# Kernel tuning notes

Hardware: AMD Instinct MI355X
Metric: run time of the kernel (lower is better)

The kernel has to match this reference:

```python
import jax, jax.numpy as jnp
import numpy as np

N = 50000      # nodes
E = 800000     # edges (avg degree 16)
D = 128        # node_dim
H = 128        # hidden_dim
ED = 16        # edge_dim (unused by GCNConv, kept for signature fidelity)
G = 64         # graphs in batch
EPS = 1e-5     # BatchNorm eps


def setup_inputs() -> dict:
    key = jax.random.key(0)
    ks = jax.random.split(key, 16)
    s = 0.05
    inp = {
        "x": jax.random.normal(ks[0], (N, D), jnp.float32),
        "edge_index": jax.random.randint(ks[1], (2, E), 0, N, dtype=jnp.int64),
        "edge_attr": jax.random.normal(ks[2], (E, ED), jnp.float32),
        "batch": jnp.sort(jax.random.randint(ks[3], (N,), 0, G, dtype=jnp.int64)),
        # GCNConv weights/biases
        "W1": jax.random.normal(ks[4], (D, H), jnp.float32) * s,
        "b1": jnp.zeros((H,), jnp.float32),
        "W2": jax.random.normal(ks[5], (H, H), jnp.float32) * s,
        "b2": jnp.zeros((H,), jnp.float32),
        "W3": jax.random.normal(ks[6], (H, H), jnp.float32) * s,
        "b3": jnp.zeros((H,), jnp.float32),
        # BatchNorm affine params (training-mode batch stats)
        "g1": jnp.ones((H,), jnp.float32), "be1": jnp.zeros((H,), jnp.float32),
        "g2": jnp.ones((H,), jnp.float32), "be2": jnp.zeros((H,), jnp.float32),
        "g3": jnp.ones((H,), jnp.float32), "be3": jnp.zeros((H,), jnp.float32),
    }
    return inp


def reference(x, edge_index, edge_attr, batch,
              W1, b1, W2, b2, W3, b3,
              g1, be1, g2, be2, g3, be3):
    n = x.shape[0]
    src, dst = edge_index[0], edge_index[1]

    # GCN symmetric normalization with added self-loops:
    # deg[i] = 1 + in_degree(i); norm(e) = deg[src]^-1/2 * deg[dst]^-1/2
    deg = jax.ops.segment_sum(jnp.ones((src.shape[0],), x.dtype), dst,
                              num_segments=n) + 1.0
    dinv = jax.lax.rsqrt(deg)
    edge_norm = (dinv[src] * dinv[dst])[:, None]   # [E,1]
    self_norm = (dinv * dinv)[:, None]             # [N,1] self-loop weight

    def gcn(h, W, b):
        h = h @ W                                  # [N,H]
        agg = jax.ops.segment_sum(h[src] * edge_norm, dst, num_segments=n)
        return agg + h * self_norm + b

    def bn_sigmoid(h, g, b):
        m = h.mean(0)
        v = jnp.mean(jnp.square(h - m), 0)         # biased variance (torch BN)
        return jax.nn.sigmoid((h - m) * jax.lax.rsqrt(v + EPS) * g + b)

    h = bn_sigmoid(gcn(x, W1, b1), g1, be1)
    h = bn_sigmoid(gcn(h, W2, b2), g2, be2)
    h = bn_sigmoid(gcn(h, W3, b3), g3, be3)

    # global_mean_pool over graph ids
    cnt = jax.ops.segment_sum(jnp.ones((n,), h.dtype), batch, num_segments=G)
    pooled = jax.ops.segment_sum(h, batch, num_segments=G)
    return pooled / jnp.maximum(cnt, 1.0)[:, None]
```

## Files before the change

### kernel.cpp

```cpp
#include <hip/hip_runtime.h>
#include <math.h>

#define NDIM 128

typedef __attribute__((ext_vector_type(8))) short short8;
typedef __attribute__((ext_vector_type(4))) float f32x4;

__device__ __forceinline__ float sigmoidf_(float x){ return 1.0f/(1.0f + __expf(-x)); }

__device__ __forceinline__ unsigned short f2bf(float f){
  unsigned u = __float_as_uint(f);
  unsigned r = (u + 0x7fffu + ((u >> 16) & 1u)) >> 16;
  return (unsigned short)r;
}

__global__ void deg_count_k(const int* __restrict__ dst, int* __restrict__ counts, int E){
  int e = blockIdx.x*blockDim.x + threadIdx.x;
  if(e < E) atomicAdd(&counts[dst[e]], 1);
}

__global__ void scan1_k(const int* __restrict__ counts, int* __restrict__ scanned,
                        int* __restrict__ chunksums, int N){
  __shared__ int lds[256];
  int t = threadIdx.x; int idx = blockIdx.x*256 + t;
  int x = (idx < N) ? counts[idx] : 0;
  lds[t] = x; __syncthreads();
  for(int o=1;o<256;o<<=1){
    int v = (t>=o) ? lds[t-o] : 0;
    __syncthreads();
    lds[t] += v;
    __syncthreads();
  }
  if(idx < N) scanned[idx] = lds[t];
  if(t == 255) chunksums[blockIdx.x] = lds[255];
}

__global__ void scan2_k(int* __restrict__ chunksums, int nchunks){
  __shared__ int lds[256];
  int t = threadIdx.x;
  int x = (t < nchunks) ? chunksums[t] : 0;
  lds[t] = x; __syncthreads();
  for(int o=1;o<256;o<<=1){
    int v = (t>=o) ? lds[t-o] : 0;
    __syncthreads();
    lds[t] += v;
    __syncthreads();
  }
  if(t < nchunks) chunksums[t] = lds[t] - x;
}

__global__ void scan3_k(const int* __restrict__ scanned, const int* __restrict__ counts,
                        const int* __restrict__ chunksums, int* __restrict__ row_start,
                        float* __restrict__ dinv, int N){
  int i = blockIdx.x*blockDim.x + threadIdx.x;
  if(i < N){
    row_start[i] = scanned[i] - counts[i] + chunksums[i>>8];
    dinv[i] = rsqrtf(1.0f + (float)counts[i]);
  }
}

__global__ void fill_k(const int* __restrict__ src, const int* __restrict__ dst,
                       const int* __restrict__ row_start,
                       int* __restrict__ cursor, unsigned short* __restrict__ csr, int E){
  int e = blockIdx.x*blockDim.x + threadIdx.x;
  if(e >= E) return;
  int d = dst[e];
  int pos = row_start[d] + atomicAdd(&cursor[d], 1);
  csr[pos] = (unsigned short)src[e];
}

__global__ void wprep_k(const float* __restrict__ W0, const float* __restrict__ W1,
                        const float* __restrict__ W2, unsigned short* __restrict__ Wsw,
                        const int* __restrict__ batch, int* __restrict__ bound,
                        int N, int G){
  int t = blockIdx.x*256 + threadIdx.x;
  if(t < 3*16384){
    int l = t >> 14; int i = t & 16383;
    const float* W = (l==0) ? W0 : ((l==1) ? W1 : W2);
    int k = i >> 7, n = i & 127;
    Wsw[l*16384 + (((k>>3)*128 + n)<<3) + (k&7)] = f2bf(W[k*128+n]);
  } else {
    int g = t - 3*16384;
    if(g <= G){
      int lo = 0, hi = N;
      while(lo < hi){ int mid = (lo+hi)>>1; if(batch[mid] < g) lo = mid+1; else hi = mid; }
      bound[g] = lo;
    }
  }
}

__global__ __launch_bounds__(256) void gemm_mfma_k(const float* __restrict__ A,
                                                   const unsigned short* __restrict__ Wsw,
                                                   unsigned short* __restrict__ Bh,
                                                   const float* __restrict__ dinv,
                                                   const float* __restrict__ sums,
                                                   const float* __restrict__ sumsq,
                                                   const float* __restrict__ gam,
                                                   const float* __restrict__ bet,
                                                   int N){
  __shared__ unsigned short Al[16384];
  __shared__ unsigned short Wl[16384];
  __shared__ float scl[NDIM], shl[NDIM], dvl[NDIM];
  int t = threadIdx.x;
  int row0 = blockIdx.x * 128;
  bool bn = (sums != nullptr);

  if(bn && t < NDIM){
    float invN = 1.0f/(float)N;
    float m = sums[t]*invN;
    float var = fmaxf(sumsq[t]*invN - m*m, 0.f);
    float s = gam[t]*rsqrtf(var + 1e-5f);
    scl[t] = s; shl[t] = bet[t] - m*s;
  }
  __syncthreads();

  if(t < NDIM){
    int r = row0 + t;
    dvl[t] = (r < N) ? dinv[r] : 0.f;
  }
  #pragma unroll
  for(int i=0;i<8;i++){
    int u = t + i*256;
    *(uint4*)&Wl[u<<3] = *(const uint4*)&Wsw[u<<3];
  }
  int o = t & 15, rbase = t >> 4;
  #pragma unroll
  for(int it=0; it<8; it++){
    int r = rbase + it*16;
    int grow = row0 + r;
    float4 v0 = make_float4(0.f,0.f,0.f,0.f), v1 = v0;
    if(grow < N){
      v0 = *(const float4*)&A[grow*NDIM + o*8];
      v1 = *(const float4*)&A[grow*NDIM + o*8 + 4];
      if(bn){
        float4 sc0 = *(const float4*)&scl[o*8],   sh0 = *(const float4*)&shl[o*8];
        float4 sc1 = *(const float4*)&scl[o*8+4], sh1 = *(const float4*)&shl[o*8+4];
        v0.x = sigmoidf_(v0.x*sc0.x + sh0.x); v0.y = sigmoidf_(v0.y*sc0.y + sh0.y);
        v0.z = sigmoidf_(v0.z*sc0.z + sh0.z); v0.w = sigmoidf_(v0.w*sc0.w + sh0.w);
        v1.x = sigmoidf_(v1.x*sc1.x + sh1.x); v1.y = sigmoidf_(v1.y*sc1.y + sh1.y);
        v1.z = sigmoidf_(v1.z*sc1.z + sh1.z); v1.w = sigmoidf_(v1.w*sc1.w + sh1.w);
      }
    }
    uint4 pk;
    pk.x = (unsigned)f2bf(v0.x) | ((unsigned)f2bf(v0.y)<<16);
    pk.y = (unsigned)f2bf(v0.z) | ((unsigned)f2bf(v0.w)<<16);
    pk.z = (unsigned)f2bf(v1.x) | ((unsigned)f2bf(v1.y)<<16);
    pk.w = (unsigned)f2bf(v1.z) | ((unsigned)f2bf(v1.w)<<16);
    *(uint4*)&Al[(o*128 + r)<<3] = pk;
  }
  __syncthreads();

  int wv = t >> 6, lane = t & 63, quad = lane >> 4, l16 = lane & 15;
  int rw = (wv & 1) * 64, cw = (wv >> 1) * 64;
  f32x4 acc[4][4];
  #pragma unroll
  for(int rt=0;rt<4;rt++)
    #pragma unroll
    for(int ct=0;ct<4;ct++) acc[rt][ct] = (f32x4){0.f,0.f,0.f,0.f};

  #pragma unroll
  for(int ks=0; ks<4; ks++){
    short8 a[4], b[4];
    #pragma unroll
    for(int rt=0;rt<4;rt++)
      a[rt] = *(short8*)&Al[(((ks*4+quad)*128) + rw + rt*16 + l16) << 3];
    #pragma unroll
    for(int ct=0;ct<4;ct++)
      b[ct] = *(short8*)&Wl[(((ks*4+quad)*128) + cw + ct*16 + l16) << 3];
    #pragma unroll
    for(int rt=0;rt<4;rt++)
      #pragma unroll
      for(int ct=0;ct<4;ct++)
        acc[rt][ct] = __builtin_amdgcn_mfma_f32_16x16x32_bf16(a[rt], b[ct], acc[rt][ct], 0, 0, 0);
  }

  #pragma unroll
  for(int rt=0;rt<4;rt++){
    int lr = rw + rt*16 + quad*4;
    int gr = row0 + lr;
    #pragma unroll
    for(int reg=0;reg<4;reg++){
      float dv = dvl[lr + reg];
      if(gr + reg < N){
        #pragma unroll
        for(int ct=0;ct<4;ct++){
          int col = cw + ct*16 + l16;
          Bh[(gr+reg)*NDIM + col] = f2bf(acc[rt][ct][reg]*dv);
        }
      }
    }
  }
}

__global__ void agg_k(const unsigned int* __restrict__ hb,
                      const float* __restrict__ dinv,
                      const int* __restrict__ row_start, const int* __restrict__ counts,
                      const unsigned short* __restrict__ csr,
                      const float* __restrict__ bias, float* __restrict__ hC, int N){
  int i = blockIdx.x;
  if(i >= N) return;
  int lane = threadIdx.x;
  int rs = row_start[i], re = rs + counts[i];
  float ax = 0.f, ay = 0.f;
  int j = rs;
  for(; j+7 < re; j += 8){
    int s0=csr[j],   s1=csr[j+1], s2=csr[j+2], s3=csr[j+3];
    int s4=csr[j+4], s5=csr[j+5], s6=csr[j+6], s7=csr[j+7];
    unsigned u0 = hb[(size_t)s0*64 + lane];
    unsigned u1 = hb[(size_t)s1*64 + lane];
    unsigned u2 = hb[(size_t)s2*64 + lane];
    unsigned u3 = hb[(size_t)s3*64 + lane];
    unsigned u4 = hb[(size_t)s4*64 + lane];
    unsigned u5 = hb[(size_t)s5*64 + lane];
    unsigned u6 = hb[(size_t)s6*64 + lane];
    unsigned u7 = hb[(size_t)s7*64 + lane];
    ax += __uint_as_float(u0<<16) + __uint_as_float(u1<<16)
        + __uint_as_float(u2<<16) + __uint_as_float(u3<<16)
        + __uint_as_float(u4<<16) + __uint_as_float(u5<<16)
        + __uint_as_float(u6<<16) + __uint_as_float(u7<<16);
    ay += __uint_as_float(u0 & 0xffff0000u) + __uint_as_float(u1 & 0xffff0000u)
        + __uint_as_float(u2 & 0xffff0000u) + __uint_as_float(u3 & 0xffff0000u)
        + __uint_as_float(u4 & 0xffff0000u) + __uint_as_float(u5 & 0xffff0000u)
        + __uint_as_float(u6 & 0xffff0000u) + __uint_as_float(u7 & 0xffff0000u);
  }
  for(; j < re; j++){
    int s0 = csr[j];
    unsigned u0 = hb[(size_t)s0*64 + lane];
    ax += __uint_as_float(u0<<16);
    ay += __uint_as_float(u0 & 0xffff0000u);
  }
  float di = dinv[i];
  unsigned su = hb[(size_t)i*64 + lane];
  float2 bv = *(const float2*)&bias[lane*2];
  float2 o;
  o.x = di*(ax + __uint_as_float(su<<16))           + bv.x;
  o.y = di*(ay + __uint_as_float(su & 0xffff0000u)) + bv.y;
  *(float2*)&hC[(size_t)i*NDIM + lane*2] = o;
}

__global__ void stats_k(const float* __restrict__ h, float* __restrict__ sums,
                        float* __restrict__ sumsq, int N){
  __shared__ float ls[256], lq[256];
  int t = threadIdx.x;
  int f = t & 127, half = t >> 7;
  int rowsPerBlock = (N + gridDim.x - 1)/gridDim.x;
  int r0 = blockIdx.x * rowsPerBlock;
  int r1 = min(N, r0 + rowsPerBlock);
  float s=0.f, q=0.f;
  for(int r=r0+half; r<r1; r+=2){
    float v = h[r*NDIM + f];
    s += v; q += v*v;
  }
  ls[t]=s; lq[t]=q; __syncthreads();
  if(t < 128){
    s = ls[t] + ls[t+128];
    q = lq[t] + lq[t+128];
    atomicAdd(&sums[f], s);
    atomicAdd(&sumsq[f], q);
  }
}

#define PCH 128
__global__ __launch_bounds__(256) void pool_k(const float* __restrict__ hC,
                                              const int* __restrict__ batch,
                                              const float* __restrict__ sums,
                                              const float* __restrict__ sumsq,
                                              const float* __restrict__ gam,
                                              const float* __restrict__ bet,
                                              float* __restrict__ out, int N){
  __shared__ float scl[NDIM], shl[NDIM];
  int t = threadIdx.x;
  if(t < NDIM){
    float invN = 1.0f/(float)N;
    float m = sums[t]*invN;
    float var = fmaxf(sumsq[t]*invN - m*m, 0.f);
    float s = gam[t]*rsqrtf(var + 1e-5f);
    scl[t] = s; shl[t] = bet[t] - m*s;
  }
  __syncthreads();
  int f = t & 127, half = t >> 7;
  int r0 = blockIdx.x*PCH + half;
  int r1 = min(N, blockIdx.x*PCH + PCH);
  float sc = scl[f], sh = shl[f];
  float acc = 0.f; int cur = -1;
  for(int r = r0; r < r1; r += 2){
    int g = batch[r];
    if(g != cur){
      if(cur >= 0) atomicAdd(&out[cur*NDIM + f], acc);
      acc = 0.f; cur = g;
    }
    acc += sigmoidf_(hC[r*NDIM + f]*sc + sh);
  }
  if(cur >= 0) atomicAdd(&out[cur*NDIM + f], acc);
}

__global__ void div_k(float* __restrict__ out, const int* __restrict__ bound){
  int g = blockIdx.x, f = threadIdx.x;
  float cnt = (float)(bound[g+1] - bound[g]);
  out[g*NDIM + f] /= fmaxf(cnt, 1.0f);
}

extern "C" void kernel_launch(void* const* d_in, const int* in_sizes, int n_in,
                              void* d_out, int out_size, void* d_ws, size_t ws_size,
                              hipStream_t stream){
  const float* x     = (const float*)d_in[0];
  const int*   ei    = (const int*)d_in[1];
  const int*   batch = (const int*)d_in[3];
  const float* W [3] = {(const float*)d_in[4], (const float*)d_in[6], (const float*)d_in[8]};
  const float* bi[3] = {(const float*)d_in[5], (const float*)d_in[7], (const float*)d_in[9]};
  const float* gg[3] = {(const float*)d_in[10], (const float*)d_in[12], (const float*)d_in[14]};
  const float* bb[3] = {(const float*)d_in[11], (const float*)d_in[13], (const float*)d_in[15]};

  int N = in_sizes[0] / NDIM;
  int E = in_sizes[1] / 2;
  int G = out_size / NDIM;
  const int* src = ei;
  const int* dst = ei + E;

  char* p = (char*)d_ws;
  auto alloc = [&](size_t bytes)->void*{
    void* r = (void*)p; p += (bytes + 255) & ~(size_t)255; return r;
  };
  unsigned short* hB  = (unsigned short*)alloc((size_t)N*NDIM*2);
  unsigned short* Wsw = (unsigned short*)alloc(3*16384*2);
  float* hC        = (float*)alloc((size_t)N*NDIM*4);
  int*   counts    = (int*)  alloc((size_t)2*N*4);
  int*   cursor    = counts + N;
  int*   scanned   = (int*)  alloc((size_t)N*4);
  int*   chunksums = (int*)  alloc(256*4);
  int*   row_start = (int*)  alloc((size_t)N*4);
  float* dinv      = (float*)alloc((size_t)N*4);
  unsigned short* csr = (unsigned short*)alloc((size_t)E*2);
  float* sums      = (float*)alloc(2*3*128*4);
  float* sumsq     = sums + 3*128;
  int*   bound     = (int*)  alloc(256*4);

  hipMemsetAsync(counts, 0, (size_t)2*N*4, stream);
  hipMemsetAsync(sums,  0, 2*3*128*4, stream);
  hipMemsetAsync(d_out, 0, (size_t)out_size*4, stream);

  deg_count_k<<<(E+255)/256, 256, 0, stream>>>(dst, counts, E);

  int nchunks = (N+255)/256;
  scan1_k<<<nchunks, 256, 0, stream>>>(counts, scanned, chunksums, N);
  scan2_k<<<1, 256, 0, stream>>>(chunksums, nchunks);
  scan3_k<<<(N+255)/256, 256, 0, stream>>>(scanned, counts, chunksums, row_start, dinv, N);
  fill_k<<<(E+255)/256, 256, 0, stream>>>(src, dst, row_start, cursor, csr, E);
  wprep_k<<<(3*16384+256+255)/256, 256, 0, stream>>>(W[0], W[1], W[2], Wsw, batch, bound, N, G);

  const float* hin = x;
  for(int l=0; l<3; l++){
    const float* sm = (l == 0) ? nullptr : (sums  + (l-1)*128);
    const float* sq = (l == 0) ? nullptr : (sumsq + (l-1)*128);
    const float* gm = (l == 0) ? nullptr : gg[l-1];
    const float* be = (l == 0) ? nullptr : bb[l-1];
    gemm_mfma_k<<<(N+127)/128, 256, 0, stream>>>(hin, Wsw + l*16384, hB, dinv,
                                                 sm, sq, gm, be, N);
    agg_k<<<N, 64, 0, stream>>>((const unsigned int*)hB, dinv, row_start, counts,
                                csr, bi[l], hC, N);
    stats_k<<<400, 256, 0, stream>>>(hC, sums + l*128, sumsq + l*128, N);
    hin = hC;
  }

  pool_k<<<(N+PCH-1)/PCH, 256, 0, stream>>>(hC, batch, sums + 2*128, sumsq + 2*128,
                                            gg[2], bb[2], (float*)d_out, N);
  div_k<<<G, 128, 0, stream>>>((float*)d_out, bound);
}
```

Before: 475.7 us.

## Store aggregated activations as bf16 and build CSR with precomputed edge ranks

The aggregation output hC changes from fp32 to packed bf16, which halves the bytes written by agg_k and read by stats_k, gemm (layers 2-3) and pool_k. CSR construction now records each edge's atomic rank during degree counting, so the fill pass writes directly without a second atomic on a cursor array. This costs an extra E-sized rank buffer, and the pre-BatchNorm values lose precision, which affects the batch statistics and the downstream results.

```diff
diff --git a/kernel.cpp b/kernel.cpp
--- a/kernel.cpp
+++ b/kernel.cpp
@@ -13,10 +13,13 @@
   unsigned r = (u + 0x7fffu + ((u >> 16) & 1u)) >> 16;
   return (unsigned short)r;
 }
-
-__global__ void deg_count_k(const int* __restrict__ dst, int* __restrict__ counts, int E){
+__device__ __forceinline__ float bflo(unsigned u){ return __uint_as_float(u<<16); }
+__device__ __forceinline__ float bfhi(unsigned u){ return __uint_as_float(u & 0xffff0000u); }
+
+__global__ void pass1_k(const int* __restrict__ dst, int* __restrict__ counts,
+                        int* __restrict__ rank, int E){
   int e = blockIdx.x*blockDim.x + threadIdx.x;
-  if(e < E) atomicAdd(&counts[dst[e]], 1);
+  if(e < E) rank[e] = atomicAdd(&counts[dst[e]], 1);
 }
 
 __global__ void scan1_k(const int* __restrict__ counts, int* __restrict__ scanned,
@@ -59,14 +62,12 @@
   }
 }
 
-__global__ void fill_k(const int* __restrict__ src, const int* __restrict__ dst,
-                       const int* __restrict__ row_start,
-                       int* __restrict__ cursor, unsigned short* __restrict__ csr, int E){
+__global__ void pass2_k(const int* __restrict__ src, const int* __restrict__ dst,
+                        const int* __restrict__ rank, const int* __restrict__ row_start,
+                        unsigned short* __restrict__ csr, int E){
   int e = blockIdx.x*blockDim.x + threadIdx.x;
   if(e >= E) return;
-  int d = dst[e];
-  int pos = row_start[d] + atomicAdd(&cursor[d], 1);
-  csr[pos] = (unsigned short)src[e];
+  csr[row_start[dst[e]] + rank[e]] = (unsigned short)src[e];
 }
 
 __global__ void wprep_k(const float* __restrict__ W0, const float* __restrict__ W1,
@@ -89,7 +90,7 @@
   }
 }
 
-__global__ __launch_bounds__(256) void gemm_mfma_k(const float* __restrict__ A,
+__global__ __launch_bounds__(256) void gemm_mfma_k(const void* __restrict__ Avoid,
                                                    const unsigned short* __restrict__ Wsw,
                                                    unsigned short* __restrict__ Bh,
                                                    const float* __restrict__ dinv,
@@ -112,8 +113,6 @@
     float s = gam[t]*rsqrtf(var + 1e-5f);
     scl[t] = s; shl[t] = bet[t] - m*s;
   }
-  __syncthreads();
-
   if(t < NDIM){
     int r = row0 + t;
     dvl[t] = (r < N) ? dinv[r] : 0.f;
@@ -123,30 +122,53 @@
     int u = t + i*256;
     *(uint4*)&Wl[u<<3] = *(const uint4*)&Wsw[u<<3];
   }
+  __syncthreads();
+
   int o = t & 15, rbase = t >> 4;
-  #pragma unroll
-  for(int it=0; it<8; it++){
-    int r = rbase + it*16;
-    int grow = row0 + r;
-    float4 v0 = make_float4(0.f,0.f,0.f,0.f), v1 = v0;
-    if(grow < N){
-      v0 = *(const float4*)&A[grow*NDIM + o*8];
-      v1 = *(const float4*)&A[grow*NDIM + o*8 + 4];
-      if(bn){
-        float4 sc0 = *(const float4*)&scl[o*8],   sh0 = *(const float4*)&shl[o*8];
-        float4 sc1 = *(const float4*)&scl[o*8+4], sh1 = *(const float4*)&shl[o*8+4];
-        v0.x = sigmoidf_(v0.x*sc0.x + sh0.x); v0.y = sigmoidf_(v0.y*sc0.y + sh0.y);
-        v0.z = sigmoidf_(v0.z*sc0.z + sh0.z); v0.w = sigmoidf_(v0.w*sc0.w + sh0.w);
-        v1.x = sigmoidf_(v1.x*sc1.x + sh1.x); v1.y = sigmoidf_(v1.y*sc1.y + sh1.y);
-        v1.z = sigmoidf_(v1.z*sc1.z + sh1.z); v1.w = sigmoidf_(v1.w*sc1.w + sh1.w);
+  if(bn){
+    const unsigned* Ab = (const unsigned*)Avoid;
+    #pragma unroll
+    for(int it=0; it<8; it++){
+      int r = rbase + it*16;
+      int grow = row0 + r;
+      uint4 pk = {0,0,0,0};
+      if(grow < N){
+        uint4 pb = *(const uint4*)&Ab[(size_t)grow*64 + o*4];
+        float a0=bflo(pb.x), a1=bfhi(pb.x), a2=bflo(pb.y), a3=bfhi(pb.y);
+        float a4=bflo(pb.z), a5=bfhi(pb.z), a6=bflo(pb.w), a7=bfhi(pb.w);
+        int f = o*8;
+        a0 = sigmoidf_(a0*scl[f+0] + shl[f+0]);
+        a1 = sigmoidf_(a1*scl[f+1] + shl[f+1]);
+        a2 = sigmoidf_(a2*scl[f+2] + shl[f+2]);
+        a3 = sigmoidf_(a3*scl[f+3] + shl[f+3]);
+        a4 = sigmoidf_(a4*scl[f+4] + shl[f+4]);
+        a5 = sigmoidf_(a5*scl[f+5] + shl[f+5]);
+        a6 = sigmoidf_(a6*scl[f+6] + shl[f+6]);
+        a7 = sigmoidf_(a7*scl[f+7] + shl[f+7]);
+        pk.x = (unsigned)f2bf(a0) | ((unsigned)f2bf(a1)<<16);
+        pk.y = (unsigned)f2bf(a2) | ((unsigned)f2bf(a3)<<16);
+        pk.z = (unsigned)f2bf(a4) | ((unsigned)f2bf(a5)<<16);
+        pk.w = (unsigned)f2bf(a6) | ((unsigned)f2bf(a7)<<16);
       }
-    }
-    uint4 pk;
-    pk.x = (unsigned)f2bf(v0.x) | ((unsigned)f2bf(v0.y)<<16);
-    pk.y = (unsigned)f2bf(v0.z) | ((unsigned)f2bf(v0.w)<<16);
-    pk.z = (unsigned)f2bf(v1.x) | ((unsigned)f2bf(v1.y)<<16);
-    pk.w = (unsigned)f2bf(v1.z) | ((unsigned)f2bf(v1.w)<<16);
-    *(uint4*)&Al[(o*128 + r)<<3] = pk;
+      *(uint4*)&Al[(o*128 + r)<<3] = pk;
+    }
+  } else {
+    const float* A = (const float*)Avoid;
+    #pragma unroll
+    for(int it=0; it<8; it++){
+      int r = rbase + it*16;
+      int grow = row0 + r;
+      uint4 pk = {0,0,0,0};
+      if(grow < N){
+        float4 v0 = *(const float4*)&A[(size_t)grow*NDIM + o*8];
+        float4 v1 = *(const float4*)&A[(size_t)grow*NDIM + o*8 + 4];
+        pk.x = (unsigned)f2bf(v0.x) | ((unsigned)f2bf(v0.y)<<16);
+        pk.y = (unsigned)f2bf(v0.z) | ((unsigned)f2bf(v0.w)<<16);
+        pk.z = (unsigned)f2bf(v1.x) | ((unsigned)f2bf(v1.y)<<16);
+        pk.w = (unsigned)f2bf(v1.z) | ((unsigned)f2bf(v1.w)<<16);
+      }
+      *(uint4*)&Al[(o*128 + r)<<3] = pk;
+    }
   }
   __syncthreads();
 
@@ -185,7 +207,7 @@
         #pragma unroll
         for(int ct=0;ct<4;ct++){
           int col = cw + ct*16 + l16;
-          Bh[(gr+reg)*NDIM + col] = f2bf(acc[rt][ct][reg]*dv);
+          Bh[(size_t)(gr+reg)*NDIM + col] = f2bf(acc[rt][ct][reg]*dv);
         }
       }
     }
@@ -196,7 +218,7 @@
                       const float* __restrict__ dinv,
                       const int* __restrict__ row_start, const int* __restrict__ counts,
                       const unsigned short* __restrict__ csr,
-                      const float* __restrict__ bias, float* __restrict__ hC, int N){
+                      const float* __restrict__ bias, unsigned int* __restrict__ hCb, int N){
   int i = blockIdx.x;
   if(i >= N) return;
   int lane = threadIdx.x;
@@ -214,31 +236,23 @@
     unsigned u5 = hb[(size_t)s5*64 + lane];
     unsigned u6 = hb[(size_t)s6*64 + lane];
     unsigned u7 = hb[(size_t)s7*64 + lane];
-    ax += __uint_as_float(u0<<16) + __uint_as_float(u1<<16)
-        + __uint_as_float(u2<<16) + __uint_as_float(u3<<16)
-        + __uint_as_float(u4<<16) + __uint_as_float(u5<<16)
-        + __uint_as_float(u6<<16) + __uint_as_float(u7<<16);
-    ay += __uint_as_float(u0 & 0xffff0000u) + __uint_as_float(u1 & 0xffff0000u)
-        + __uint_as_float(u2 & 0xffff0000u) + __uint_as_float(u3 & 0xffff0000u)
-        + __uint_as_float(u4 & 0xffff0000u) + __uint_as_float(u5 & 0xffff0000u)
-        + __uint_as_float(u6 & 0xffff0000u) + __uint_as_float(u7 & 0xffff0000u);
+    ax += bflo(u0)+bflo(u1)+bflo(u2)+bflo(u3)+bflo(u4)+bflo(u5)+bflo(u6)+bflo(u7);
+    ay += bfhi(u0)+bfhi(u1)+bfhi(u2)+bfhi(u3)+bfhi(u4)+bfhi(u5)+bfhi(u6)+bfhi(u7);
   }
   for(; j < re; j++){
-    int s0 = csr[j];
-    unsigned u0 = hb[(size_t)s0*64 + lane];
-    ax += __uint_as_float(u0<<16);
-    ay += __uint_as_float(u0 & 0xffff0000u);
+    unsigned u0 = hb[(size_t)csr[j]*64 + lane];
+    ax += bflo(u0);
+    ay += bfhi(u0);
   }
   float di = dinv[i];
   unsigned su = hb[(size_t)i*64 + lane];
   float2 bv = *(const float2*)&bias[lane*2];
-  float2 o;
-  o.x = di*(ax + __uint_as_float(su<<16))           + bv.x;
-  o.y = di*(ay + __uint_as_float(su & 0xffff0000u)) + bv.y;
-  *(float2*)&hC[(size_t)i*NDIM + lane*2] = o;
-}
-
-__global__ void stats_k(const float* __restrict__ h, float* __restrict__ sums,
+  float ox = di*(ax + bflo(su)) + bv.x;
+  float oy = di*(ay + bfhi(su)) + bv.y;
+  hCb[(size_t)i*64 + lane] = (unsigned)f2bf(ox) | ((unsigned)f2bf(oy)<<16);
+}
+
+__global__ void stats_k(const unsigned* __restrict__ hb, float* __restrict__ sums,
                         float* __restrict__ sumsq, int N){
   __shared__ float ls[256], lq[256];
   int t = threadIdx.x;
@@ -248,7 +262,8 @@
   int r1 = min(N, r0 + rowsPerBlock);
   float s=0.f, q=0.f;
   for(int r=r0+half; r<r1; r+=2){
-    float v = h[r*NDIM + f];
+    unsigned u = hb[(size_t)r*64 + (f>>1)];
+    float v = (f&1) ? bfhi(u) : bflo(u);
     s += v; q += v*v;
   }
   ls[t]=s; lq[t]=q; __syncthreads();
@@ -261,7 +276,7 @@
 }
 
 #define PCH 128
-__global__ __launch_bounds__(256) void pool_k(const float* __restrict__ hC,
+__global__ __launch_bounds__(256) void pool_k(const unsigned* __restrict__ hb,
                                               const int* __restrict__ batch,
                                               const float* __restrict__ sums,
                                               const float* __restrict__ sumsq,
@@ -289,7 +304,9 @@
       if(cur >= 0) atomicAdd(&out[cur*NDIM + f], acc);
       acc = 0.f; cur = g;
     }
-    acc += sigmoidf_(hC[r*NDIM + f]*sc + sh);
+    unsigned u = hb[(size_t)r*64 + (f>>1)];
+    float v = (f&1) ? bfhi(u) : bflo(u);
+    acc += sigmoidf_(v*sc + sh);
   }
   if(cur >= 0) atomicAdd(&out[cur*NDIM + f], acc);
 }
@@ -322,10 +339,10 @@
     void* r = (void*)p; p += (bytes + 255) & ~(size_t)255; return r;
   };
   unsigned short* hB  = (unsigned short*)alloc((size_t)N*NDIM*2);
+  unsigned*       hCb = (unsigned*)      alloc((size_t)N*64*4);
   unsigned short* Wsw = (unsigned short*)alloc(3*16384*2);
-  float* hC        = (float*)alloc((size_t)N*NDIM*4);
-  int*   counts    = (int*)  alloc((size_t)2*N*4);
-  int*   cursor    = counts + N;
+  int*   counts    = (int*)  alloc((size_t)N*4);
+  int*   rank      = (int*)  alloc((size_t)E*4);
   int*   scanned   = (int*)  alloc((size_t)N*4);
   int*   chunksums = (int*)  alloc(256*4);
   int*   row_start = (int*)  alloc((size_t)N*4);
@@ -335,20 +352,20 @@
   float* sumsq     = sums + 3*128;
   int*   bound     = (int*)  alloc(256*4);
 
-  hipMemsetAsync(counts, 0, (size_t)2*N*4, stream);
+  hipMemsetAsync(counts, 0, (size_t)N*4, stream);
   hipMemsetAsync(sums,  0, 2*3*128*4, stream);
   hipMemsetAsync(d_out, 0, (size_t)out_size*4, stream);
 
-  deg_count_k<<<(E+255)/256, 256, 0, stream>>>(dst, counts, E);
+  pass1_k<<<(E+255)/256, 256, 0, stream>>>(dst, counts, rank, E);
 
   int nchunks = (N+255)/256;
   scan1_k<<<nchunks, 256, 0, stream>>>(counts, scanned, chunksums, N);
   scan2_k<<<1, 256, 0, stream>>>(chunksums, nchunks);
   scan3_k<<<(N+255)/256, 256, 0, stream>>>(scanned, counts, chunksums, row_start, dinv, N);
-  fill_k<<<(E+255)/256, 256, 0, stream>>>(src, dst, row_start, cursor, csr, E);
+  pass2_k<<<(E+255)/256, 256, 0, stream>>>(src, dst, rank, row_start, csr, E);
   wprep_k<<<(3*16384+256+255)/256, 256, 0, stream>>>(W[0], W[1], W[2], Wsw, batch, bound, N, G);
 
-  const float* hin = x;
+  const void* hin = (const void*)x;
   for(int l=0; l<3; l++){
     const float* sm = (l == 0) ? nullptr : (sums  + (l-1)*128);
     const float* sq = (l == 0) ? nullptr : (sumsq + (l-1)*128);
@@ -357,12 +374,12 @@
     gemm_mfma_k<<<(N+127)/128, 256, 0, stream>>>(hin, Wsw + l*16384, hB, dinv,
                                                  sm, sq, gm, be, N);
     agg_k<<<N, 64, 0, stream>>>((const unsigned int*)hB, dinv, row_start, counts,
-                                csr, bi[l], hC, N);
-    stats_k<<<400, 256, 0, stream>>>(hC, sums + l*128, sumsq + l*128, N);
-    hin = hC;
-  }
-
-  pool_k<<<(N+PCH-1)/PCH, 256, 0, stream>>>(hC, batch, sums + 2*128, sumsq + 2*128,
+                                csr, bi[l], hCb, N);
+    stats_k<<<400, 256, 0, stream>>>(hCb, sums + l*128, sumsq + l*128, N);
+    hin = (const void*)hCb;
+  }
+
+  pool_k<<<(N+PCH-1)/PCH, 256, 0, stream>>>(hCb, batch, sums + 2*128, sumsq + 2*128,
                                             gg[2], bb[2], (float*)d_out, N);
   div_k<<<G, 128, 0, stream>>>((float*)d_out, bound);
 }
```

New measurement: 448.9 us. -5.6%, faster.
